# Kernel optimization log

Hardware: AMD Instinct MI355X
Metric: run time of the kernel (lower is better)

Reference implementation:

```python
import jax, jax.numpy as jnp
import numpy as np

N, D, K = 32768, 128, 16
EPS = 1e-8  # torch cosine_similarity eps


def setup_inputs() -> dict:
    key = jax.random.key(0)
    k1, k2, kW1, kW2, kV = jax.random.split(key, 5)
    # xavier_normal std for [K, fan_in, fan_out]-style tensors (torch treats dim0 as batch? no:
    # xavier_normal_ on a 3D tensor uses fan_in = D*1? torch computes fan from dims 1.. with receptive field.
    # fan_in = size(1)*rf, fan_out = size(0)*rf where rf = prod(shape[2:]).
    def xavier_std(shape):
        rf = int(np.prod(shape[2:])) if len(shape) > 2 else 1
        fan_in = shape[1] * rf
        fan_out = shape[0] * rf
        return float(np.sqrt(2.0 / (fan_in + fan_out)))
    W1 = jax.random.normal(kW1, (K, D, D), jnp.float32) * xavier_std((K, D, D))
    W2 = jax.random.normal(kW2, (K, D, D), jnp.float32) * xavier_std((K, D, D))
    V = jax.random.normal(kV, (K, 2 * D, 1), jnp.float32) * xavier_std((K, 2 * D, 1))
    b = jnp.zeros((K,), jnp.float32)
    x_1 = jax.random.normal(k1, (N, D), jnp.float32)
    x_2 = jax.random.normal(k2, (N, D), jnp.float32)
    return {"x_1": x_1, "x_2": x_2, "W1": W1, "W2": W2, "V": V, "b": b}


def reference(x_1, x_2, W1, W2, V, b):
    # Batched version of the per-slice loop: one bmm per side instead of K matmuls.
    x1_t = jnp.einsum('nd,kde->kne', x_1, W1)  # [K, N, D]
    x2_t = jnp.einsum('nd,kde->kne', x_2, W2)  # [K, N, D]
    # torch.cosine_similarity(dim=-1): dot / (clamp(||a||, eps) * clamp(||b||, eps))
    num = jnp.sum(x1_t * x2_t, axis=-1)                      # [K, N]
    n1 = jnp.maximum(jnp.sqrt(jnp.sum(x1_t * x1_t, -1)), EPS)
    n2 = jnp.maximum(jnp.sqrt(jnp.sum(x2_t * x2_t, -1)), EPS)
    part1 = num / (n1 * n2)                                  # [K, N]
    x_cat = jnp.concatenate([x_1, x_2], axis=-1)             # [N, 2D]
    part2 = jnp.einsum('nc,kc->kn', x_cat, V[:, :, 0])       # [K, N]
    fea = part1 + part2 + b[:, None]                         # [K, N]
    return jax.nn.relu(fea.T)                                # [N, K]
```

## Files before the change

kernel.cpp:

```cpp
#include <hip/hip_runtime.h>


typedef __attribute__((ext_vector_type(8))) __bf16 bf16x8;
typedef __attribute__((ext_vector_type(8))) unsigned short us8;
typedef __attribute__((ext_vector_type(4))) float f32x4;

static __device__ __forceinline__ unsigned short f2bf(float f) {
  unsigned u = __float_as_uint(f);
  u += 0x7FFFu + ((u >> 16) & 1u);
  return (unsigned short)(u >> 16);
}

static __device__ __forceinline__ bf16x8 as_bf(us8 u) {
  bf16x8 r;
  __builtin_memcpy(&r, &u, sizeof(r));
  return r;
}

__global__ void ntn_prep(const float* __restrict__ W1, const float* __restrict__ W2,
                         const float* __restrict__ V,
                         unsigned short* __restrict__ wsW, unsigned short* __restrict__ wsV) {
  int e2 = blockIdx.x * 256 + threadIdx.x;
  if (e2 < 524288) {
    int j = e2 & 7, t = e2 >> 3;
    int u = t & 2047, cc = t >> 11;
    int lane = u & 63, s = (u >> 6) & 3, et2 = (u >> 8) & 3, side = (u >> 10) & 1;
    int h = cc & 1, k = cc >> 1;
    int q = lane >> 4, l15 = lane & 15;
    int et = h * 4 + et2;
    const float* W = side ? W2 : W1;
    wsW[e2] = f2bf(W[k * 16384 + (s * 32 + q * 8 + j) * 128 + (et * 16 + l15)]);
  } else if (e2 < 528384) {
    int v2 = e2 - 524288;
    int j = v2 & 7, u = v2 >> 3;
    int lane = u & 63, cs = u >> 6;
    int q = lane >> 4, l15 = lane & 15;
    wsV[v2] = f2bf(V[l15 * 256 + cs * 32 + q * 8 + j]);
  }
}

__global__ __launch_bounds__(256, 2) void ntn_main(
    const float* __restrict__ x1, const float* __restrict__ x2,
    const float* __restrict__ b,
    const unsigned short* __restrict__ wsW, const unsigned short* __restrict__ wsV,
    float* __restrict__ out) {
  __shared__ uint4 ldsW[2][2048];

  const int tid = threadIdx.x;
  const int lane = tid & 63, wave = tid >> 6;
  const int q = lane >> 4, l15 = lane & 15;
  const int kh = blockIdx.x & 1;
  const int rb = blockIdx.x >> 1;
  const int rowbase = rb * 128 + wave * 32;

  const f32x4 zero4 = {0.f, 0.f, 0.f, 0.f};

  auto stage = [&](int cc, int slot) {
    const unsigned short* src = wsW + (size_t)cc * 16384 + (size_t)(wave * 512 + lane) * 8;
    uint4* dst = &ldsW[slot][wave * 512];
#pragma unroll
    for (int i = 0; i < 8; ++i)
      __builtin_amdgcn_global_load_lds(
          (__attribute__((address_space(1))) void*)(void*)(src + i * 512),
          (__attribute__((address_space(3))) void*)(dst + i * 64), 16, 0, 0);
  };

  stage(kh * 16, 0);

  bf16x8 xb[2][2][4];
#pragma unroll
  for (int side = 0; side < 2; ++side) {
    const float* xp0 = side ? x2 : x1;
#pragma unroll
    for (int nt = 0; nt < 2; ++nt) {
#pragma unroll
      for (int s = 0; s < 4; ++s) {
        const float* p = xp0 + (size_t)(rowbase + nt * 16 + l15) * 128 + s * 32 + q * 8;
        float4 v0 = *(const float4*)p;
        float4 v1 = *(const float4*)(p + 4);
        us8 uu;
        uu[0] = f2bf(v0.x); uu[1] = f2bf(v0.y); uu[2] = f2bf(v0.z); uu[3] = f2bf(v0.w);
        uu[4] = f2bf(v1.x); uu[5] = f2bf(v1.y); uu[6] = f2bf(v1.z); uu[7] = f2bf(v1.w);
        xb[side][nt][s] = as_bf(uu);
      }
    }
  }

  f32x4 accP[2];
  {
    bf16x8 vf[8];
#pragma unroll
    for (int cs = 0; cs < 8; ++cs)
      vf[cs] = as_bf(*(const us8*)(wsV + (size_t)(cs * 64 + lane) * 8));
    float4 bv = *(const float4*)(b + q * 4);
#pragma unroll
    for (int nt = 0; nt < 2; ++nt) {
      f32x4 a = zero4;
#pragma unroll
      for (int cs = 0; cs < 8; ++cs)
        a = __builtin_amdgcn_mfma_f32_16x16x32_bf16(vf[cs], xb[cs >> 2][nt][cs & 3], a, 0, 0, 0);
      a.x += bv.x; a.y += bv.y; a.z += bv.z; a.w += bv.w;
      accP[nt] = a;
    }
  }

  float nm[2] = {0.f, 0.f}, q1[2] = {0.f, 0.f}, q2[2] = {0.f, 0.f};

  auto compute = [&](int slot) {
#pragma unroll
    for (int et = 0; et < 4; ++et) {
      bf16x8 wa[4], wb[4];
#pragma unroll
      for (int s = 0; s < 4; ++s) {
        wa[s] = as_bf(*(const us8*)&ldsW[slot][et * 256 + s * 64 + lane]);
        wb[s] = as_bf(*(const us8*)&ldsW[slot][1024 + et * 256 + s * 64 + lane]);
      }
#pragma unroll
      for (int nt = 0; nt < 2; ++nt) {
        f32x4 a1 = zero4, a2 = zero4;
#pragma unroll
        for (int s = 0; s < 4; ++s)
          a1 = __builtin_amdgcn_mfma_f32_16x16x32_bf16(wa[s], xb[0][nt][s], a1, 0, 0, 0);
#pragma unroll
        for (int s = 0; s < 4; ++s)
          a2 = __builtin_amdgcn_mfma_f32_16x16x32_bf16(wb[s], xb[1][nt][s], a2, 0, 0, 0);
        nm[nt] += a1.x * a2.x + a1.y * a2.y + a1.z * a2.z + a1.w * a2.w;
        q1[nt] += a1.x * a1.x + a1.y * a1.y + a1.z * a1.z + a1.w * a1.w;
        q2[nt] += a2.x * a2.x + a2.y * a2.y + a2.z * a2.z + a2.w * a2.w;
      }
    }
  };

#pragma unroll 1
  for (int kk = 0; kk < 8; ++kk) {
    const int cbase = kh * 16 + 2 * kk;
    __syncthreads();
    stage(cbase + 1, 1);
    compute(0);
    __syncthreads();
    if (kk < 7) stage(cbase + 2, 0);
    compute(1);

    const int k = kh * 8 + kk;
    const int qo = k >> 2;
    const int r  = k & 3;
#pragma unroll
    for (int nt = 0; nt < 2; ++nt) {
      float n = nm[nt], s1 = q1[nt], s2 = q2[nt];
      n  += __shfl_xor(n, 16);  n  += __shfl_xor(n, 32);
      s1 += __shfl_xor(s1, 16); s1 += __shfl_xor(s1, 32);
      s2 += __shfl_xor(s2, 16); s2 += __shfl_xor(s2, 32);
      float d1 = fmaxf(sqrtf(s1), 1e-8f);
      float d2 = fmaxf(sqrtf(s2), 1e-8f);
      float p1 = n / (d1 * d2);
      float pc = (r == 0) ? accP[nt].x : (r == 1) ? accP[nt].y
               : (r == 2) ? accP[nt].z : accP[nt].w;
      if (q == qo)
        out[(size_t)(rowbase + nt * 16 + l15) * 16 + k] = fmaxf(p1 + pc, 0.f);
      nm[nt] = 0.f; q1[nt] = 0.f; q2[nt] = 0.f;
    }
  }
}

extern "C" void kernel_launch(void* const* d_in, const int* in_sizes, int n_in,
                              void* d_out, int out_size, void* d_ws, size_t ws_size,
                              hipStream_t stream) {
  const float* x1 = (const float*)d_in[0];
  const float* x2 = (const float*)d_in[1];
  const float* W1 = (const float*)d_in[2];
  const float* W2 = (const float*)d_in[3];
  const float* V  = (const float*)d_in[4];
  const float* b  = (const float*)d_in[5];
  float* out = (float*)d_out;
  unsigned short* wsW = (unsigned short*)d_ws;
  unsigned short* wsV = wsW + (size_t)65536 * 8;

  ntn_prep<<<2064, 256, 0, stream>>>(W1, W2, V, wsW, wsV);
  ntn_main<<<512, 256, 0, stream>>>(x1, x2, b, wsW, wsV, out);
}
```

Measured before the change: 119.4 us.

## Stagger weight-chunk order and LDS fragment order, double-buffer fragments, pack FMAs

Several changes at once. Neighbouring blocks now walk the k slices in a rotated order so they stop fetching the same weight chunk together, and each wave starts at a different et tile so LDS reads from different waves spread out. LDS fragment loads are double-buffered so the next tile loads while the current MFMAs run, and the norm/dot accumulators use packed float2 math. Launch bounds drop to one block per SIMD-pair, which frees registers for the extra fragment buffers but may lower occupancy.

```diff
diff --git a/kernel.cpp b/kernel.cpp
--- a/kernel.cpp
+++ b/kernel.cpp
@@ -4,6 +4,7 @@
 typedef __attribute__((ext_vector_type(8))) __bf16 bf16x8;
 typedef __attribute__((ext_vector_type(8))) unsigned short us8;
 typedef __attribute__((ext_vector_type(4))) float f32x4;
+typedef __attribute__((ext_vector_type(2))) float f32x2;
 
 static __device__ __forceinline__ unsigned short f2bf(float f) {
   unsigned u = __float_as_uint(f);
@@ -39,7 +40,7 @@
   }
 }
 
-__global__ __launch_bounds__(256, 2) void ntn_main(
+__global__ __launch_bounds__(256, 1) void ntn_main(
     const float* __restrict__ x1, const float* __restrict__ x2,
     const float* __restrict__ b,
     const unsigned short* __restrict__ wsW, const unsigned short* __restrict__ wsV,
@@ -52,6 +53,7 @@
   const int kh = blockIdx.x & 1;
   const int rb = blockIdx.x >> 1;
   const int rowbase = rb * 128 + wave * 32;
+  const int par = (blockIdx.x >> 1) & 1;
 
   const f32x4 zero4 = {0.f, 0.f, 0.f, 0.f};
 
@@ -65,7 +67,8 @@
           (__attribute__((address_space(3))) void*)(dst + i * 64), 16, 0, 0);
   };
 
-  stage(kh * 16, 0);
+  const int kk0 = par * 4;
+  stage(kh * 16 + 2 * kk0, 0);
 
   bf16x8 xb[2][2][4];
 #pragma unroll
@@ -104,41 +107,59 @@
     }
   }
 
-  float nm[2] = {0.f, 0.f}, q1[2] = {0.f, 0.f}, q2[2] = {0.f, 0.f};
+  f32x2 nmv[2], q1v[2], q2v[2];
+#pragma unroll
+  for (int nt = 0; nt < 2; ++nt) {
+    nmv[nt] = (f32x2){0.f, 0.f}; q1v[nt] = (f32x2){0.f, 0.f}; q2v[nt] = (f32x2){0.f, 0.f};
+  }
+
+  auto ldfr = [&](int slot, int et, bf16x8 (&wa)[4], bf16x8 (&wb)[4]) {
+#pragma unroll
+    for (int s = 0; s < 4; ++s) {
+      wa[s] = as_bf(*(const us8*)&ldsW[slot][et * 256 + s * 64 + lane]);
+      wb[s] = as_bf(*(const us8*)&ldsW[slot][1024 + et * 256 + s * 64 + lane]);
+    }
+  };
+
+  const int e0 = wave & 3;
 
   auto compute = [&](int slot) {
-#pragma unroll
-    for (int et = 0; et < 4; ++et) {
-      bf16x8 wa[4], wb[4];
-#pragma unroll
-      for (int s = 0; s < 4; ++s) {
-        wa[s] = as_bf(*(const us8*)&ldsW[slot][et * 256 + s * 64 + lane]);
-        wb[s] = as_bf(*(const us8*)&ldsW[slot][1024 + et * 256 + s * 64 + lane]);
-      }
+    bf16x8 waA[4], wbA[4], waB[4], wbB[4];
+    ldfr(slot, e0, waA, wbA);
+#pragma unroll
+    for (int ei = 0; ei < 4; ++ei) {
+      bf16x8 (&wac)[4] = (ei & 1) ? waB : waA;
+      bf16x8 (&wbc)[4] = (ei & 1) ? wbB : wbA;
+      bf16x8 (&wan)[4] = (ei & 1) ? waA : waB;
+      bf16x8 (&wbn)[4] = (ei & 1) ? wbA : wbB;
+      if (ei < 3) ldfr(slot, (e0 + ei + 1) & 3, wan, wbn);
 #pragma unroll
       for (int nt = 0; nt < 2; ++nt) {
         f32x4 a1 = zero4, a2 = zero4;
 #pragma unroll
         for (int s = 0; s < 4; ++s)
-          a1 = __builtin_amdgcn_mfma_f32_16x16x32_bf16(wa[s], xb[0][nt][s], a1, 0, 0, 0);
+          a1 = __builtin_amdgcn_mfma_f32_16x16x32_bf16(wac[s], xb[0][nt][s], a1, 0, 0, 0);
 #pragma unroll
         for (int s = 0; s < 4; ++s)
-          a2 = __builtin_amdgcn_mfma_f32_16x16x32_bf16(wb[s], xb[1][nt][s], a2, 0, 0, 0);
-        nm[nt] += a1.x * a2.x + a1.y * a2.y + a1.z * a2.z + a1.w * a2.w;
-        q1[nt] += a1.x * a1.x + a1.y * a1.y + a1.z * a1.z + a1.w * a1.w;
-        q2[nt] += a2.x * a2.x + a2.y * a2.y + a2.z * a2.z + a2.w * a2.w;
+          a2 = __builtin_amdgcn_mfma_f32_16x16x32_bf16(wbc[s], xb[1][nt][s], a2, 0, 0, 0);
+        f32x2 a1lo = {a1.x, a1.y}, a1hi = {a1.z, a1.w};
+        f32x2 a2lo = {a2.x, a2.y}, a2hi = {a2.z, a2.w};
+        nmv[nt] += a1lo * a2lo; nmv[nt] += a1hi * a2hi;
+        q1v[nt] += a1lo * a1lo; q1v[nt] += a1hi * a1hi;
+        q2v[nt] += a2lo * a2lo; q2v[nt] += a2hi * a2hi;
       }
     }
   };
 
 #pragma unroll 1
-  for (int kk = 0; kk < 8; ++kk) {
+  for (int i = 0; i < 8; ++i) {
+    const int kk = (kk0 + i) & 7;
     const int cbase = kh * 16 + 2 * kk;
     __syncthreads();
     stage(cbase + 1, 1);
     compute(0);
     __syncthreads();
-    if (kk < 7) stage(cbase + 2, 0);
+    if (i < 7) stage(kh * 16 + 2 * ((kk0 + i + 1) & 7), 0);
     compute(1);
 
     const int k = kh * 8 + kk;
@@ -146,7 +167,9 @@
     const int r  = k & 3;
 #pragma unroll
     for (int nt = 0; nt < 2; ++nt) {
-      float n = nm[nt], s1 = q1[nt], s2 = q2[nt];
+      float n = nmv[nt].x + nmv[nt].y;
+      float s1 = q1v[nt].x + q1v[nt].y;
+      float s2 = q2v[nt].x + q2v[nt].y;
       n  += __shfl_xor(n, 16);  n  += __shfl_xor(n, 32);
       s1 += __shfl_xor(s1, 16); s1 += __shfl_xor(s1, 32);
       s2 += __shfl_xor(s2, 16); s2 += __shfl_xor(s2, 32);
@@ -157,7 +180,7 @@
                : (r == 2) ? accP[nt].z : accP[nt].w;
       if (q == qo)
         out[(size_t)(rowbase + nt * 16 + l15) * 16 + k] = fmaxf(p1 + pc, 0.f);
-      nm[nt] = 0.f; q1[nt] = 0.f; q2[nt] = 0.f;
+      nmv[nt] = (f32x2){0.f, 0.f}; q1v[nt] = (f32x2){0.f, 0.f}; q2v[nt] = (f32x2){0.f, 0.f};
     }
   }
 }
```

After: 134.8 us. 12.9% more time.
